# Performance work log

Measured on AMD Instinct MI355X. Metric: run time of the kernel, lower is better.

Reference implementation:

```python
import jax, jax.numpy as jnp
import numpy as np

B, N, FD, HD, G = 32, 512, 768, 384, 3
ALPHA = 0.2  # LeakyReLU slope
NEG = -9e15


def layer_norm(x, g, b, eps=1e-5):
    m = jnp.mean(x, axis=-1, keepdims=True)
    v = jnp.var(x, axis=-1, keepdims=True)
    return (x - m) / jnp.sqrt(v + eps) * g + b


def gat_layer(x, adj, W, a):
    # x: [B,N,FD], adj: [N,N], W: [FD,HD], a: [2*HD]
    h = jnp.einsum('bnf,fd->bnd', x, W)  # [B,N,HD]
    # concat score decomposes: e_ij = lrelu(h_i . a[:HD] + h_j . a[HD:])
    e1 = h @ a[:HD]   # [B,N]
    e2 = h @ a[HD:]   # [B,N]
    e = jax.nn.leaky_relu(e1[:, :, None] + e2[:, None, :], ALPHA)  # [B,N,N]
    e = jnp.where(adj[None] > 0, e, NEG)
    att = jax.nn.softmax(e, axis=2)  # masked softmax over neighbors
    h_prime = jnp.einsum('bij,bjd->bid', att, h)
    return jax.nn.elu(h_prime)  # concat=True -> ELU


def setup_inputs() -> dict:
    key = jax.random.key(0)
    ks = jax.random.split(key, 10)
    s = 0.05
    return {
        'x': jax.random.normal(ks[0], (B, N, FD), jnp.float32),
        'adj': jax.random.randint(ks[1], (G, N, N), 0, 2),
        'W': jax.random.normal(ks[2], (G, FD, HD), jnp.float32) * s,
        'a': jax.random.normal(ks[3], (G, 2 * HD), jnp.float32) * s,
        'log_unc': jnp.zeros((G,), jnp.float32),
        'gate_w': jax.random.normal(ks[4], (FD, G), jnp.float32) * s,
        'gate_b': jnp.zeros((G,), jnp.float32),
        'ln1_g': jnp.ones((HD,), jnp.float32),
        'ln1_b': jnp.zeros((HD,), jnp.float32),
        'w1': jax.random.normal(ks[5], (HD, HD), jnp.float32) * s,
        'b1': jnp.zeros((HD,), jnp.float32),
        'w2': jax.random.normal(ks[6], (HD, FD), jnp.float32) * s,
        'b2': jnp.zeros((FD,), jnp.float32),
        'ln2_g': jnp.ones((FD,), jnp.float32),
        'ln2_b': jnp.zeros((FD,), jnp.float32),
    }


def reference(x, adj, W, a, log_unc, gate_w, gate_b, ln1_g, ln1_b,
              w1, b1, w2, b2, ln2_g, ln2_b):
    # global (uncertainty) weights
    unc = jnp.exp(log_unc)
    attw = jax.nn.softmax(1.0 / (unc + 1e-8))  # [G]
    # content gates from batch-averaged features
    avg = jnp.mean(x, axis=0)                          # [N,FD]
    cg = jax.nn.softmax(avg @ gate_w + gate_b, axis=-1)  # [N,G]
    # per-graph GAT + LayerNorm, vmapped over the G graphs
    gouts = jax.vmap(lambda ad, Wi, ai: layer_norm(gat_layer(x, ad, Wi, ai), ln1_g, ln1_b))(adj, W, a)  # [G,B,N,HD]
    weights = 0.7 * attw[:, None, None, None] + 0.3 * cg.T[:, None, :, None]  # [G,1|B,N,1]
    fused = jnp.sum(weights * gouts, axis=0)  # [B,N,HD]
    # output projection + LayerNorm
    proj = jax.nn.relu(fused @ w1 + b1) @ w2 + b2
    proj = layer_norm(proj, ln2_g, ln2_b)
    # residual gate
    gv = jax.nn.sigmoid(jnp.sum(proj * x, axis=-1, keepdims=True) / np.sqrt(FD).astype(np.float32))
    return gv * x + (1.0 - gv) * proj
```

## Files before the change

### kernel.cpp

```cpp
#include <hip/hip_runtime.h>

typedef unsigned short ushort_t;
typedef unsigned int uint_t;
typedef __bf16 bf16x8 __attribute__((ext_vector_type(8)));
typedef float f32x4 __attribute__((ext_vector_type(4)));
typedef unsigned int u32x4 __attribute__((ext_vector_type(4)));
typedef unsigned short u16x4 __attribute__((ext_vector_type(4)));

#define B_SZ 32
#define N_SZ 512
#define FD_SZ 768
#define HD_SZ 384
#define G_SZ 3
#define M_SZ (B_SZ * N_SZ)
#define ALPHA_LR 0.2f
#define NEGV -9.0e15f
#define VTILE (HD_SZ * 32)

__device__ __forceinline__ float bf2f(ushort_t u) { return __uint_as_float(((uint_t)u) << 16); }
__device__ __forceinline__ ushort_t f2bf(float f) {
  uint_t x = __float_as_uint(f);
  return (ushort_t)((x + 0x7fffu + ((x >> 16) & 1u)) >> 16);
}
__device__ __forceinline__ u32x4 pack8(f32x4 lo, f32x4 hi) {
  union { ushort_t us[8]; u32x4 v; } pk;
  pk.us[0] = f2bf(lo.x); pk.us[1] = f2bf(lo.y); pk.us[2] = f2bf(lo.z); pk.us[3] = f2bf(lo.w);
  pk.us[4] = f2bf(hi.x); pk.us[5] = f2bf(hi.y); pk.us[6] = f2bf(hi.z); pk.us[7] = f2bf(hi.w);
  return pk.v;
}

__global__ __launch_bounds__(256) void transpose_f2b(
    const float* __restrict__ src, ushort_t* __restrict__ dst, int R, int C) {
  size_t total = (size_t)R * C;
  size_t base = (size_t)blockIdx.z * total;
  size_t i = (size_t)blockIdx.x * 256 + threadIdx.x;
  if (i < total) {
    int r = (int)(i / C), c = (int)(i % C);
    dst[base + (size_t)c * R + r] = f2bf(src[base + i]);
  }
}

__global__ __launch_bounds__(256) void cast_f2b(
    const float* __restrict__ src, ushort_t* __restrict__ dst) {
  size_t i = (size_t)blockIdx.x * 256 + threadIdx.x;
  f32x4 v = ((const f32x4*)src)[i];
  u16x4 p;
  p[0] = f2bf(v.x); p[1] = f2bf(v.y); p[2] = f2bf(v.z); p[3] = f2bf(v.w);
  ((u16x4*)dst)[i] = p;
}

__global__ __launch_bounds__(256) void pack_adj(
    const int* __restrict__ adj, uint_t* __restrict__ am) {
  size_t i = (size_t)blockIdx.x * 256 + threadIdx.x;
  unsigned long long mask = __ballot(adj[i] != 0);
  int lane = threadIdx.x & 63;
  if ((lane & 31) == 0) am[i >> 5] = (uint_t)(mask >> (lane & 32));
}

__global__ __launch_bounds__(256) void gate_kernel(
    const float* __restrict__ x, const float* __restrict__ gate_w,
    const float* __restrict__ gate_b, float* __restrict__ cg) {
  int n = blockIdx.x;
  int tid = threadIdx.x;
  float a0 = 0.f, a1 = 0.f, a2 = 0.f;
  for (int f = tid; f < FD_SZ; f += 256) {
    float s = 0.f;
#pragma unroll
    for (int b = 0; b < B_SZ; b++) s += x[((size_t)b * N_SZ + n) * FD_SZ + f];
    float avg = s * (1.0f / B_SZ);
    a0 += avg * gate_w[f * 3 + 0];
    a1 += avg * gate_w[f * 3 + 1];
    a2 += avg * gate_w[f * 3 + 2];
  }
  for (int m = 1; m < 64; m <<= 1) {
    a0 += __shfl_xor(a0, m, 64);
    a1 += __shfl_xor(a1, m, 64);
    a2 += __shfl_xor(a2, m, 64);
  }
  __shared__ float red[3][4];
  int wave = tid >> 6, lane = tid & 63;
  if (lane == 0) { red[0][wave] = a0; red[1][wave] = a1; red[2][wave] = a2; }
  __syncthreads();
  if (tid == 0) {
    float l0 = red[0][0] + red[0][1] + red[0][2] + red[0][3] + gate_b[0];
    float l1 = red[1][0] + red[1][1] + red[1][2] + red[1][3] + gate_b[1];
    float l2 = red[2][0] + red[2][1] + red[2][2] + red[2][3] + gate_b[2];
    float mx = fmaxf(l0, fmaxf(l1, l2));
    float e0 = __expf(l0 - mx), e1 = __expf(l1 - mx), e2 = __expf(l2 - mx);
    float inv = 1.0f / (e0 + e1 + e2);
    cg[n * 3 + 0] = e0 * inv;
    cg[n * 3 + 1] = e1 * inv;
    cg[n * 3 + 2] = e2 * inv;
  }
}

template <bool AF32, bool RELU, bool OUTBF16, bool HASBIAS, bool VFOUT>
__global__ __launch_bounds__(256) void gemm_kernel(
    const void* __restrict__ Av, size_t strideA,
    const ushort_t* __restrict__ Bt, size_t strideB,
    const float* __restrict__ bias,
    void* __restrict__ Cv, size_t strideC,
    int M, int K, int Nc) {
  __shared__ __attribute__((aligned(16))) ushort_t As[128 * 32];
  __shared__ __attribute__((aligned(16))) ushort_t Bs[128 * 32];
  int tid = threadIdx.x, wave = tid >> 6, lane = tid & 63;
  int m0 = blockIdx.y * 128, n0 = blockIdx.x * 128;
  const float* Abf32 = (const float*)Av + (size_t)blockIdx.z * strideA;
  const ushort_t* Abb16 = (const ushort_t*)Av + (size_t)blockIdx.z * strideA;
  const ushort_t* Bb = Bt + (size_t)blockIdx.z * strideB;

  f32x4 acc[4][4];
  f32x4 z4 = {0.f, 0.f, 0.f, 0.f};
#pragma unroll
  for (int i = 0; i < 4; i++)
#pragma unroll
    for (int j = 0; j < 4; j++) acc[i][j] = z4;

  int wm = (wave & 1) * 64, wn = (wave >> 1) * 64;
  int srow = lane >> 2, schk = (lane & 3) * 8;

  for (int kt = 0; kt < K; kt += 32) {
    u32x4 av[2], bv[2];
#pragma unroll
    for (int i = 0; i < 2; i++) {
      int row = m0 + wave * 32 + i * 16 + srow;
      if (AF32) {
        const float* ap = Abf32 + (size_t)row * K + kt + schk;
        f32x4 lo = *(const f32x4*)ap;
        f32x4 hi = *(const f32x4*)(ap + 4);
        av[i] = pack8(lo, hi);
      } else {
        av[i] = *(const u32x4*)(Abb16 + (size_t)row * K + kt + schk);
      }
      bv[i] = *(const u32x4*)(Bb + (size_t)(n0 + wave * 32 + i * 16 + srow) * K + kt + schk);
    }
    __syncthreads();
#pragma unroll
    for (int i = 0; i < 2; i++) {
      int rowBase = wave * 32 + i * 16;
      *(u32x4*)(As + rowBase * 32 + lane * 8) = av[i];
      *(u32x4*)(Bs + rowBase * 32 + lane * 8) = bv[i];
    }
    __syncthreads();
    bf16x8 af[4], bfr[4];
#pragma unroll
    for (int t = 0; t < 4; t++) {
      af[t] = *(const bf16x8*)(As + (wm + t * 16 + (lane & 15)) * 32 + (lane >> 4) * 8);
      bfr[t] = *(const bf16x8*)(Bs + (wn + t * 16 + (lane & 15)) * 32 + (lane >> 4) * 8);
    }
#pragma unroll
    for (int mt = 0; mt < 4; mt++)
#pragma unroll
      for (int nt = 0; nt < 4; nt++)
        acc[mt][nt] = __builtin_amdgcn_mfma_f32_16x16x32_bf16(af[mt], bfr[nt], acc[mt][nt], 0, 0, 0);
  }

  if (VFOUT) {
#pragma unroll
    for (int mt = 0; mt < 4; mt++) {
#pragma unroll
      for (int nt = 0; nt < 4; nt++) {
        int d = n0 + wn + nt * 16 + (lane & 15);
        int gm = m0 + wm + mt * 16 + (lane >> 4) * 4;
        int b = gm >> 9, jt = (gm >> 5) & 15, j2 = gm & 31;
        u16x4 pk;
#pragma unroll
        for (int r2 = 0; r2 < 4; r2++) pk[r2] = f2bf(acc[mt][nt][r2]);
        size_t off = ((size_t)((blockIdx.z * B_SZ + b) * 16 + jt)) * VTILE + (size_t)d * 32 + j2;
        *(u16x4*)((ushort_t*)Cv + off) = pk;
      }
    }
  } else {
#pragma unroll
    for (int mt = 0; mt < 4; mt++) {
#pragma unroll
      for (int nt = 0; nt < 4; nt++) {
        int gn = n0 + wn + nt * 16 + (lane & 15);
        float bvs = HASBIAS ? bias[gn] : 0.f;
#pragma unroll
        for (int r2 = 0; r2 < 4; r2++) {
          int gm = m0 + wm + mt * 16 + (lane >> 4) * 4 + r2;
          float v = acc[mt][nt][r2] + bvs;
          if (RELU) v = v > 0.f ? v : 0.f;
          size_t off = (size_t)blockIdx.z * strideC + (size_t)gm * Nc + gn;
          if (OUTBF16) ((ushort_t*)Cv)[off] = f2bf(v);
          else ((float*)Cv)[off] = v;
        }
      }
    }
  }
}

__global__ __launch_bounds__(256) void e12_kernel(
    const ushort_t* __restrict__ vf, const float* __restrict__ a,
    float* __restrict__ e1, float* __restrict__ e2) {
  __shared__ float a1s[HD_SZ], a2s[HD_SZ];
  int g = blockIdx.y;
  int tid = threadIdx.x;
  for (int i = tid; i < HD_SZ; i += 256) {
    a1s[i] = a[g * 2 * HD_SZ + i];
    a2s[i] = a[g * 2 * HD_SZ + HD_SZ + i];
  }
  __syncthreads();
  int m = blockIdx.x * 256 + tid;
  int b = m >> 9, jt = (m >> 5) & 15, j2 = m & 31;
  const ushort_t* col = vf + ((size_t)((g * B_SZ + b) * 16 + jt)) * VTILE + j2;
  float s1 = 0.f, s2 = 0.f;
  for (int d = 0; d < HD_SZ; d++) {
    float h = bf2f(col[d * 32]);
    s1 += h * a1s[d];
    s2 += h * a2s[d];
  }
  e1[(size_t)g * M_SZ + m] = s1;
  e2[(size_t)g * M_SZ + m] = s2;
}

__global__ __launch_bounds__(512, 4) void attn_kernel(
    const uint_t* __restrict__ adjm, const ushort_t* __restrict__ vf,
    const float* __restrict__ e1, const float* __restrict__ e2,
    const float* __restrict__ cg, const float* __restrict__ log_unc,
    const float* __restrict__ ln1g, const float* __restrict__ ln1b,
    ushort_t* __restrict__ fusedbf) {
  __shared__ __attribute__((aligned(16))) ushort_t Pb[32][520];
  __shared__ float e2s[512];
  __shared__ float e1r[32];
  __shared__ uint_t amS[32][16];
  __shared__ float lng[HD_SZ], lnb[HD_SZ];
  __shared__ float cgr[32][3];
  __shared__ float s1s[32][8], s2s[32][8];

  int tid = threadIdx.x, wave = tid >> 6, lane = tid & 63;
  int quad = lane >> 4, l15 = lane & 15;
  int L = blockIdx.x + (blockIdx.y << 4);
  int b = (L & 7) + ((L >> 7) << 3);
  int i0 = ((L >> 3) & 15) * 32;

  float iv0 = 1.f / (__expf(log_unc[0]) + 1e-8f);
  float iv1 = 1.f / (__expf(log_unc[1]) + 1e-8f);
  float iv2 = 1.f / (__expf(log_unc[2]) + 1e-8f);
  float mxa = fmaxf(iv0, fmaxf(iv1, iv2));
  float w0 = __expf(iv0 - mxa), w1 = __expf(iv1 - mxa), w2 = __expf(iv2 - mxa);
  float wsum = 1.f / (w0 + w1 + w2);
  float attw[3] = {w0 * wsum, w1 * wsum, w2 * wsum};

  if (tid < HD_SZ) {
    lng[tid] = ln1g[tid];
    lnb[tid] = ln1b[tid];
  }
  if (tid < 96) cgr[tid / 3][tid % 3] = cg[(i0 + tid / 3) * 3 + tid % 3];

  float facc[24];
#pragma unroll
  for (int t = 0; t < 24; t++) facc[t] = 0.f;

  for (int g = 0; g < G_SZ; g++) {
    __syncthreads();
    if (tid < 32) e1r[tid] = e1[((size_t)g * B_SZ + b) * N_SZ + i0 + tid];
    amS[tid >> 4][tid & 15] = adjm[((size_t)g * N_SZ + i0 + (tid >> 4)) * 16 + (tid & 15)];
    e2s[tid] = e2[((size_t)g * B_SZ + b) * N_SZ + tid];
    __syncthreads();

#pragma unroll
    for (int rr = 0; rr < 4; rr++) {
      int rw = wave * 4 + rr;
      float e1v = e1r[rw];
      float sv[8];
      float m = -3.0e38f;
#pragma unroll
      for (int jj = 0; jj < 8; jj++) {
        int j = lane + jj * 64;
        float s = e1v + e2s[j];
        s = s > 0.f ? s : ALPHA_LR * s;
        uint_t mw = amS[rw][(lane >> 5) + jj * 2];
        s = ((mw >> (j & 31)) & 1u) ? s : NEGV;
        sv[jj] = s;
        m = fmaxf(m, s);
      }
      for (int msk = 1; msk < 64; msk <<= 1) m = fmaxf(m, __shfl_xor(m, msk, 64));
      float sum = 0.f;
#pragma unroll
      for (int jj = 0; jj < 8; jj++) {
        float e = __expf(sv[jj] - m);
        sv[jj] = e;
        sum += e;
      }
      for (int msk = 1; msk < 64; msk <<= 1) sum += __shfl_xor(sum, msk, 64);
      float inv = 1.0f / sum;
#pragma unroll
      for (int jj = 0; jj < 8; jj++) Pb[rw][lane + jj * 64] = f2bf(sv[jj] * inv);
    }
    __syncthreads();

    f32x4 acc[2][3];
    f32x4 z4 = {0.f, 0.f, 0.f, 0.f};
#pragma unroll
    for (int mt = 0; mt < 2; mt++)
#pragma unroll
      for (int t = 0; t < 3; t++) acc[mt][t] = z4;
    const ushort_t* vbase = vf + ((size_t)(g * B_SZ + b) * 16) * VTILE;
#pragma unroll 2
    for (int j0 = 0; j0 < N_SZ; j0 += 32) {
      const ushort_t* vtile = vbase + (size_t)(j0 >> 5) * VTILE;
      bf16x8 af0 = *(const bf16x8*)(&Pb[l15][j0 + quad * 8]);
      bf16x8 af1 = *(const bf16x8*)(&Pb[16 + l15][j0 + quad * 8]);
#pragma unroll
      for (int t = 0; t < 3; t++) {
        bf16x8 bf = *(const bf16x8*)(vtile + (wave * 48 + t * 16 + l15) * 32 + quad * 8);
        acc[0][t] = __builtin_amdgcn_mfma_f32_16x16x32_bf16(af0, bf, acc[0][t], 0, 0, 0);
        acc[1][t] = __builtin_amdgcn_mfma_f32_16x16x32_bf16(af1, bf, acc[1][t], 0, 0, 0);
      }
    }

    float ps1[2][4], ps2[2][4];
#pragma unroll
    for (int mt = 0; mt < 2; mt++)
#pragma unroll
      for (int r = 0; r < 4; r++) { ps1[mt][r] = 0.f; ps2[mt][r] = 0.f; }
#pragma unroll
    for (int mt = 0; mt < 2; mt++)
#pragma unroll
      for (int t = 0; t < 3; t++)
#pragma unroll
        for (int r = 0; r < 4; r++) {
          float v = acc[mt][t][r];
          v = v > 0.f ? v : __expf(v) - 1.f;
          acc[mt][t][r] = v;
          ps1[mt][r] += v;
          ps2[mt][r] += v * v;
        }
#pragma unroll
    for (int msk = 1; msk < 16; msk <<= 1) {
#pragma unroll
      for (int mt = 0; mt < 2; mt++)
#pragma unroll
        for (int r = 0; r < 4; r++) {
          ps1[mt][r] += __shfl_xor(ps1[mt][r], msk, 64);
          ps2[mt][r] += __shfl_xor(ps2[mt][r], msk, 64);
        }
    }
    if (l15 == 0) {
#pragma unroll
      for (int mt = 0; mt < 2; mt++)
#pragma unroll
        for (int r = 0; r < 4; r++) {
          s1s[mt * 16 + quad * 4 + r][wave] = ps1[mt][r];
          s2s[mt * 16 + quad * 4 + r][wave] = ps2[mt][r];
        }
    }
    __syncthreads();
#pragma unroll
    for (int mt = 0; mt < 2; mt++)
#pragma unroll
      for (int r = 0; r < 4; r++) {
        int row = mt * 16 + quad * 4 + r;
        float S1 = 0.f, S2 = 0.f;
#pragma unroll
        for (int w = 0; w < 8; w++) {
          S1 += s1s[row][w];
          S2 += s2s[row][w];
        }
        float mean = S1 * (1.f / HD_SZ);
        float var = S2 * (1.f / HD_SZ) - mean * mean;
        float rs = rsqrtf(var + 1e-5f);
        float wgt = 0.7f * attw[g] + 0.3f * cgr[row][g];
#pragma unroll
        for (int t = 0; t < 3; t++) {
          int d = wave * 48 + t * 16 + l15;
          facc[mt * 12 + t * 4 + r] += wgt * ((acc[mt][t][r] - mean) * rs * lng[d] + lnb[d]);
        }
      }
  }
#pragma unroll
  for (int mt = 0; mt < 2; mt++)
#pragma unroll
    for (int r = 0; r < 4; r++) {
      size_t rowo = ((size_t)b * N_SZ + i0 + mt * 16 + quad * 4 + r) * HD_SZ;
#pragma unroll
      for (int t = 0; t < 3; t++)
        fusedbf[rowo + wave * 48 + t * 16 + l15] = f2bf(facc[mt * 12 + t * 4 + r]);
    }
}

__global__ __launch_bounds__(256) void final_kernel(
    const ushort_t* __restrict__ projbf, const float* __restrict__ x,
    const float* __restrict__ ln2g, const float* __restrict__ ln2b,
    float* __restrict__ out) {
  int row = blockIdx.x;
  int tid = threadIdx.x, wave = tid >> 6, lane = tid & 63;
  const ushort_t* pr = projbf + (size_t)row * FD_SZ;
  const float* xr = x + (size_t)row * FD_SZ;
  float v[3], xv[3];
  float s1 = 0.f, s2 = 0.f;
#pragma unroll
  for (int k = 0; k < 3; k++) {
    int c = tid + k * 256;
    v[k] = bf2f(pr[c]);
    xv[k] = xr[c];
    s1 += v[k];
    s2 += v[k] * v[k];
  }
  for (int m = 1; m < 64; m <<= 1) {
    s1 += __shfl_xor(s1, m, 64);
    s2 += __shfl_xor(s2, m, 64);
  }
  __shared__ float rs1[4], rs2[4], rdt[4];
  if (lane == 0) { rs1[wave] = s1; rs2[wave] = s2; }
  __syncthreads();
  s1 = rs1[0] + rs1[1] + rs1[2] + rs1[3];
  s2 = rs2[0] + rs2[1] + rs2[2] + rs2[3];
  float mean = s1 * (1.f / FD_SZ);
  float var = s2 * (1.f / FD_SZ) - mean * mean;
  float rstd = rsqrtf(var + 1e-5f);
  float dot = 0.f;
  float pn[3];
#pragma unroll
  for (int k = 0; k < 3; k++) {
    int c = tid + k * 256;
    pn[k] = (v[k] - mean) * rstd * ln2g[c] + ln2b[c];
    dot += pn[k] * xv[k];
  }
  for (int m = 1; m < 64; m <<= 1) dot += __shfl_xor(dot, m, 64);
  if (lane == 0) rdt[wave] = dot;
  __syncthreads();
  dot = rdt[0] + rdt[1] + rdt[2] + rdt[3];
  float gv = 1.f / (1.f + __expf(-dot * (1.0f / 27.712812921102035f)));
#pragma unroll
  for (int k = 0; k < 3; k++) {
    int c = tid + k * 256;
    out[(size_t)row * FD_SZ + c] = gv * xv[k] + (1.f - gv) * pn[k];
  }
}

extern "C" void kernel_launch(void* const* d_in, const int* in_sizes, int n_in,
                              void* d_out, int out_size, void* d_ws, size_t ws_size,
                              hipStream_t stream) {
  (void)in_sizes; (void)n_in; (void)out_size; (void)ws_size;
  const float* x = (const float*)d_in[0];
  const int* adj = (const int*)d_in[1];
  const float* W = (const float*)d_in[2];
  const float* a = (const float*)d_in[3];
  const float* log_unc = (const float*)d_in[4];
  const float* gate_w = (const float*)d_in[5];
  const float* gate_b = (const float*)d_in[6];
  const float* ln1g = (const float*)d_in[7];
  const float* ln1b = (const float*)d_in[8];
  const float* w1 = (const float*)d_in[9];
  const float* b1 = (const float*)d_in[10];
  const float* w2 = (const float*)d_in[11];
  const float* b2 = (const float*)d_in[12];
  const float* ln2g = (const float*)d_in[13];
  const float* ln2b = (const float*)d_in[14];

  char* ws = (char*)d_ws;
  ushort_t* Wt      = (ushort_t*)(ws + 0);
  uint_t*   adjm    = (uint_t*)(ws + 0);
  ushort_t* w1t     = (ushort_t*)(ws + 1769472);
  ushort_t* w2t     = (ushort_t*)(ws + 2064384);
  float*    cg      = (float*)(ws + 2654208);
  float*    e1      = (float*)(ws + 2660352);
  float*    e2      = (float*)(ws + 2856960);
  ushort_t* fusedbf = (ushort_t*)(ws + 3053568);
  ushort_t* vf      = (ushort_t*)(ws + 15636480);
  ushort_t* t1bf    = (ushort_t*)(ws + 15636480);
  ushort_t* projbf  = (ushort_t*)(ws + 28219392);
  ushort_t* xb      = (ushort_t*)d_out;

  cast_f2b<<<dim3((M_SZ * FD_SZ) / 1024), 256, 0, stream>>>(x, xb);

  transpose_f2b<<<dim3(1152, 1, 3), 256, 0, stream>>>(W, Wt, FD_SZ, HD_SZ);
  transpose_f2b<<<dim3(576, 1, 1), 256, 0, stream>>>(w1, w1t, HD_SZ, HD_SZ);
  transpose_f2b<<<dim3(1152, 1, 1), 256, 0, stream>>>(w2, w2t, HD_SZ, FD_SZ);

  gate_kernel<<<dim3(N_SZ), 256, 0, stream>>>(x, gate_w, gate_b, cg);

  gemm_kernel<false, false, true, false, true><<<dim3(3, 128, 3), 256, 0, stream>>>(
      xb, 0, Wt, (size_t)HD_SZ * FD_SZ, nullptr, vf, 0,
      M_SZ, FD_SZ, HD_SZ);

  pack_adj<<<dim3((G_SZ * N_SZ * N_SZ) / 256), 256, 0, stream>>>(adj, adjm);

  e12_kernel<<<dim3(M_SZ / 256, G_SZ), 256, 0, stream>>>(vf, a, e1, e2);

  attn_kernel<<<dim3(N_SZ / 32, B_SZ), 512, 0, stream>>>(
      adjm, vf, e1, e2, cg, log_unc, ln1g, ln1b, fusedbf);

  gemm_kernel<false, true, true, true, false><<<dim3(3, 128, 1), 256, 0, stream>>>(
      fusedbf, 0, w1t, 0, b1, t1bf, 0, M_SZ, HD_SZ, HD_SZ);
  gemm_kernel<false, false, true, true, false><<<dim3(6, 128, 1), 256, 0, stream>>>(
      t1bf, 0, w2t, 0, b2, projbf, 0, M_SZ, HD_SZ, FD_SZ);

  final_kernel<<<dim3(M_SZ), 256, 0, stream>>>(projbf, x, ln2g, ln2b, (float*)d_out);
}
```

Before: 349.0 us.

## Split attention kernel across graphs and reduce partials in a separate pass

The attention kernel now launches one block per (row tile, batch, graph) instead of looping over the three graphs inside each block. Each block writes its weighted, layer-normalised output as a bf16 partial into a per-graph slice of the output buffer, and a new kernel sums the three slices into the fused tensor. This triples the grid to raise occupancy and parallelism, at the cost of extra global memory traffic, an additional launch, and an extra bf16 rounding of each partial before the sum.

```diff
diff --git a/kernel.cpp b/kernel.cpp
--- a/kernel.cpp
+++ b/kernel.cpp
@@ -6,6 +6,7 @@
 typedef float f32x4 __attribute__((ext_vector_type(4)));
 typedef unsigned int u32x4 __attribute__((ext_vector_type(4)));
 typedef unsigned short u16x4 __attribute__((ext_vector_type(4)));
+typedef unsigned short u16x8 __attribute__((ext_vector_type(8)));
 
 #define B_SZ 32
 #define N_SZ 512
@@ -16,6 +17,7 @@
 #define ALPHA_LR 0.2f
 #define NEGV -9.0e15f
 #define VTILE (HD_SZ * 32)
+#define PSLICE ((size_t)M_SZ * HD_SZ)
 
 __device__ __forceinline__ float bf2f(ushort_t u) { return __uint_as_float(((uint_t)u) << 16); }
 __device__ __forceinline__ ushort_t f2bf(float f) {
@@ -220,17 +222,18 @@
     const float* __restrict__ e1, const float* __restrict__ e2,
     const float* __restrict__ cg, const float* __restrict__ log_unc,
     const float* __restrict__ ln1g, const float* __restrict__ ln1b,
-    ushort_t* __restrict__ fusedbf) {
+    ushort_t* __restrict__ pf) {
   __shared__ __attribute__((aligned(16))) ushort_t Pb[32][520];
   __shared__ float e2s[512];
   __shared__ float e1r[32];
   __shared__ uint_t amS[32][16];
   __shared__ float lng[HD_SZ], lnb[HD_SZ];
-  __shared__ float cgr[32][3];
+  __shared__ float cgr[32];
   __shared__ float s1s[32][8], s2s[32][8];
 
   int tid = threadIdx.x, wave = tid >> 6, lane = tid & 63;
   int quad = lane >> 4, l15 = lane & 15;
+  int g = blockIdx.z;
   int L = blockIdx.x + (blockIdx.y << 4);
   int b = (L & 7) + ((L >> 7) << 3);
   int i0 = ((L >> 3) & 15) * 32;
@@ -241,144 +244,143 @@
   float mxa = fmaxf(iv0, fmaxf(iv1, iv2));
   float w0 = __expf(iv0 - mxa), w1 = __expf(iv1 - mxa), w2 = __expf(iv2 - mxa);
   float wsum = 1.f / (w0 + w1 + w2);
-  float attw[3] = {w0 * wsum, w1 * wsum, w2 * wsum};
+  float attwg = (g == 0 ? w0 : (g == 1 ? w1 : w2)) * wsum;
 
   if (tid < HD_SZ) {
     lng[tid] = ln1g[tid];
     lnb[tid] = ln1b[tid];
   }
-  if (tid < 96) cgr[tid / 3][tid % 3] = cg[(i0 + tid / 3) * 3 + tid % 3];
-
-  float facc[24];
-#pragma unroll
-  for (int t = 0; t < 24; t++) facc[t] = 0.f;
-
-  for (int g = 0; g < G_SZ; g++) {
-    __syncthreads();
-    if (tid < 32) e1r[tid] = e1[((size_t)g * B_SZ + b) * N_SZ + i0 + tid];
-    amS[tid >> 4][tid & 15] = adjm[((size_t)g * N_SZ + i0 + (tid >> 4)) * 16 + (tid & 15)];
-    e2s[tid] = e2[((size_t)g * B_SZ + b) * N_SZ + tid];
-    __syncthreads();
-
-#pragma unroll
-    for (int rr = 0; rr < 4; rr++) {
-      int rw = wave * 4 + rr;
-      float e1v = e1r[rw];
-      float sv[8];
-      float m = -3.0e38f;
-#pragma unroll
-      for (int jj = 0; jj < 8; jj++) {
-        int j = lane + jj * 64;
-        float s = e1v + e2s[j];
-        s = s > 0.f ? s : ALPHA_LR * s;
-        uint_t mw = amS[rw][(lane >> 5) + jj * 2];
-        s = ((mw >> (j & 31)) & 1u) ? s : NEGV;
-        sv[jj] = s;
-        m = fmaxf(m, s);
-      }
-      for (int msk = 1; msk < 64; msk <<= 1) m = fmaxf(m, __shfl_xor(m, msk, 64));
-      float sum = 0.f;
-#pragma unroll
-      for (int jj = 0; jj < 8; jj++) {
-        float e = __expf(sv[jj] - m);
-        sv[jj] = e;
-        sum += e;
-      }
-      for (int msk = 1; msk < 64; msk <<= 1) sum += __shfl_xor(sum, msk, 64);
-      float inv = 1.0f / sum;
-#pragma unroll
-      for (int jj = 0; jj < 8; jj++) Pb[rw][lane + jj * 64] = f2bf(sv[jj] * inv);
-    }
-    __syncthreads();
-
-    f32x4 acc[2][3];
-    f32x4 z4 = {0.f, 0.f, 0.f, 0.f};
+  if (tid < 32) {
+    cgr[tid] = cg[(i0 + tid) * 3 + g];
+    e1r[tid] = e1[((size_t)g * B_SZ + b) * N_SZ + i0 + tid];
+  }
+  amS[tid >> 4][tid & 15] = adjm[((size_t)g * N_SZ + i0 + (tid >> 4)) * 16 + (tid & 15)];
+  e2s[tid] = e2[((size_t)g * B_SZ + b) * N_SZ + tid];
+  __syncthreads();
+
+#pragma unroll
+  for (int rr = 0; rr < 4; rr++) {
+    int rw = wave * 4 + rr;
+    float e1v = e1r[rw];
+    float sv[8];
+    float m = -3.0e38f;
+#pragma unroll
+    for (int jj = 0; jj < 8; jj++) {
+      int j = lane + jj * 64;
+      float s = e1v + e2s[j];
+      s = s > 0.f ? s : ALPHA_LR * s;
+      uint_t mw = amS[rw][(lane >> 5) + jj * 2];
+      s = ((mw >> (j & 31)) & 1u) ? s : NEGV;
+      sv[jj] = s;
+      m = fmaxf(m, s);
+    }
+    for (int msk = 1; msk < 64; msk <<= 1) m = fmaxf(m, __shfl_xor(m, msk, 64));
+    float sum = 0.f;
+#pragma unroll
+    for (int jj = 0; jj < 8; jj++) {
+      float e = __expf(sv[jj] - m);
+      sv[jj] = e;
+      sum += e;
+    }
+    for (int msk = 1; msk < 64; msk <<= 1) sum += __shfl_xor(sum, msk, 64);
+    float inv = 1.0f / sum;
+#pragma unroll
+    for (int jj = 0; jj < 8; jj++) Pb[rw][lane + jj * 64] = f2bf(sv[jj] * inv);
+  }
+  __syncthreads();
+
+  f32x4 acc[2][3];
+  f32x4 z4 = {0.f, 0.f, 0.f, 0.f};
+#pragma unroll
+  for (int mt = 0; mt < 2; mt++)
+#pragma unroll
+    for (int t = 0; t < 3; t++) acc[mt][t] = z4;
+  const ushort_t* vbase = vf + ((size_t)(g * B_SZ + b) * 16) * VTILE;
+#pragma unroll 2
+  for (int j0 = 0; j0 < N_SZ; j0 += 32) {
+    const ushort_t* vtile = vbase + (size_t)(j0 >> 5) * VTILE;
+    bf16x8 af0 = *(const bf16x8*)(&Pb[l15][j0 + quad * 8]);
+    bf16x8 af1 = *(const bf16x8*)(&Pb[16 + l15][j0 + quad * 8]);
+#pragma unroll
+    for (int t = 0; t < 3; t++) {
+      bf16x8 bf = *(const bf16x8*)(vtile + (wave * 48 + t * 16 + l15) * 32 + quad * 8);
+      acc[0][t] = __builtin_amdgcn_mfma_f32_16x16x32_bf16(af0, bf, acc[0][t], 0, 0, 0);
+      acc[1][t] = __builtin_amdgcn_mfma_f32_16x16x32_bf16(af1, bf, acc[1][t], 0, 0, 0);
+    }
+  }
+
+  float ps1[2][4], ps2[2][4];
+#pragma unroll
+  for (int mt = 0; mt < 2; mt++)
+#pragma unroll
+    for (int r = 0; r < 4; r++) { ps1[mt][r] = 0.f; ps2[mt][r] = 0.f; }
+#pragma unroll
+  for (int mt = 0; mt < 2; mt++)
+#pragma unroll
+    for (int t = 0; t < 3; t++)
+#pragma unroll
+      for (int r = 0; r < 4; r++) {
+        float v = acc[mt][t][r];
+        v = v > 0.f ? v : __expf(v) - 1.f;
+        acc[mt][t][r] = v;
+        ps1[mt][r] += v;
+        ps2[mt][r] += v * v;
+      }
+#pragma unroll
+  for (int msk = 1; msk < 16; msk <<= 1) {
 #pragma unroll
     for (int mt = 0; mt < 2; mt++)
 #pragma unroll
-      for (int t = 0; t < 3; t++) acc[mt][t] = z4;
-    const ushort_t* vbase = vf + ((size_t)(g * B_SZ + b) * 16) * VTILE;
-#pragma unroll 2
-    for (int j0 = 0; j0 < N_SZ; j0 += 32) {
-      const ushort_t* vtile = vbase + (size_t)(j0 >> 5) * VTILE;
-      bf16x8 af0 = *(const bf16x8*)(&Pb[l15][j0 + quad * 8]);
-      bf16x8 af1 = *(const bf16x8*)(&Pb[16 + l15][j0 + quad * 8]);
+      for (int r = 0; r < 4; r++) {
+        ps1[mt][r] += __shfl_xor(ps1[mt][r], msk, 64);
+        ps2[mt][r] += __shfl_xor(ps2[mt][r], msk, 64);
+      }
+  }
+  if (l15 == 0) {
+#pragma unroll
+    for (int mt = 0; mt < 2; mt++)
+#pragma unroll
+      for (int r = 0; r < 4; r++) {
+        s1s[mt * 16 + quad * 4 + r][wave] = ps1[mt][r];
+        s2s[mt * 16 + quad * 4 + r][wave] = ps2[mt][r];
+      }
+  }
+  __syncthreads();
+#pragma unroll
+  for (int mt = 0; mt < 2; mt++)
+#pragma unroll
+    for (int r = 0; r < 4; r++) {
+      int row = mt * 16 + quad * 4 + r;
+      float S1 = 0.f, S2 = 0.f;
+#pragma unroll
+      for (int w = 0; w < 8; w++) {
+        S1 += s1s[row][w];
+        S2 += s2s[row][w];
+      }
+      float mean = S1 * (1.f / HD_SZ);
+      float var = S2 * (1.f / HD_SZ) - mean * mean;
+      float rs = rsqrtf(var + 1e-5f);
+      float wgt = 0.7f * attwg + 0.3f * cgr[row];
+      size_t rowo = (size_t)g * PSLICE + ((size_t)b * N_SZ + i0 + row) * HD_SZ;
 #pragma unroll
       for (int t = 0; t < 3; t++) {
-        bf16x8 bf = *(const bf16x8*)(vtile + (wave * 48 + t * 16 + l15) * 32 + quad * 8);
-        acc[0][t] = __builtin_amdgcn_mfma_f32_16x16x32_bf16(af0, bf, acc[0][t], 0, 0, 0);
-        acc[1][t] = __builtin_amdgcn_mfma_f32_16x16x32_bf16(af1, bf, acc[1][t], 0, 0, 0);
-      }
-    }
-
-    float ps1[2][4], ps2[2][4];
-#pragma unroll
-    for (int mt = 0; mt < 2; mt++)
-#pragma unroll
-      for (int r = 0; r < 4; r++) { ps1[mt][r] = 0.f; ps2[mt][r] = 0.f; }
-#pragma unroll
-    for (int mt = 0; mt < 2; mt++)
-#pragma unroll
-      for (int t = 0; t < 3; t++)
-#pragma unroll
-        for (int r = 0; r < 4; r++) {
-          float v = acc[mt][t][r];
-          v = v > 0.f ? v : __expf(v) - 1.f;
-          acc[mt][t][r] = v;
-          ps1[mt][r] += v;
-          ps2[mt][r] += v * v;
-        }
-#pragma unroll
-    for (int msk = 1; msk < 16; msk <<= 1) {
-#pragma unroll
-      for (int mt = 0; mt < 2; mt++)
-#pragma unroll
-        for (int r = 0; r < 4; r++) {
-          ps1[mt][r] += __shfl_xor(ps1[mt][r], msk, 64);
-          ps2[mt][r] += __shfl_xor(ps2[mt][r], msk, 64);
-        }
-    }
-    if (l15 == 0) {
-#pragma unroll
-      for (int mt = 0; mt < 2; mt++)
-#pragma unroll
-        for (int r = 0; r < 4; r++) {
-          s1s[mt * 16 + quad * 4 + r][wave] = ps1[mt][r];
-          s2s[mt * 16 + quad * 4 + r][wave] = ps2[mt][r];
-        }
-    }
-    __syncthreads();
-#pragma unroll
-    for (int mt = 0; mt < 2; mt++)
-#pragma unroll
-      for (int r = 0; r < 4; r++) {
-        int row = mt * 16 + quad * 4 + r;
-        float S1 = 0.f, S2 = 0.f;
-#pragma unroll
-        for (int w = 0; w < 8; w++) {
-          S1 += s1s[row][w];
-          S2 += s2s[row][w];
-        }
-        float mean = S1 * (1.f / HD_SZ);
-        float var = S2 * (1.f / HD_SZ) - mean * mean;
-        float rs = rsqrtf(var + 1e-5f);
-        float wgt = 0.7f * attw[g] + 0.3f * cgr[row][g];
-#pragma unroll
-        for (int t = 0; t < 3; t++) {
-          int d = wave * 48 + t * 16 + l15;
-          facc[mt * 12 + t * 4 + r] += wgt * ((acc[mt][t][r] - mean) * rs * lng[d] + lnb[d]);
-        }
-      }
-  }
-#pragma unroll
-  for (int mt = 0; mt < 2; mt++)
-#pragma unroll
-    for (int r = 0; r < 4; r++) {
-      size_t rowo = ((size_t)b * N_SZ + i0 + mt * 16 + quad * 4 + r) * HD_SZ;
-#pragma unroll
-      for (int t = 0; t < 3; t++)
-        fusedbf[rowo + wave * 48 + t * 16 + l15] = f2bf(facc[mt * 12 + t * 4 + r]);
-    }
+        int d = wave * 48 + t * 16 + l15;
+        pf[rowo + d] = f2bf(wgt * ((acc[mt][t][r] - mean) * rs * lng[d] + lnb[d]));
+      }
+    }
+}
+
+__global__ __launch_bounds__(256) void reduce3_kernel(
+    const ushort_t* __restrict__ pf, ushort_t* __restrict__ fused) {
+  size_t u = ((size_t)blockIdx.x * 256 + threadIdx.x) * 8;
+  u16x8 a = *(const u16x8*)(pf + u);
+  u16x8 b = *(const u16x8*)(pf + PSLICE + u);
+  u16x8 c = *(const u16x8*)(pf + 2 * PSLICE + u);
+  u16x8 o;
+#pragma unroll
+  for (int k = 0; k < 8; k++)
+    o[k] = f2bf(bf2f(a[k]) + bf2f(b[k]) + bf2f(c[k]));
+  *(u16x8*)(fused + u) = o;
 }
 
 __global__ __launch_bounds__(256) void final_kernel(
@@ -464,6 +466,7 @@
   ushort_t* t1bf    = (ushort_t*)(ws + 15636480);
   ushort_t* projbf  = (ushort_t*)(ws + 28219392);
   ushort_t* xb      = (ushort_t*)d_out;
+  ushort_t* pf      = (ushort_t*)d_out;
 
   cast_f2b<<<dim3((M_SZ * FD_SZ) / 1024), 256, 0, stream>>>(x, xb);
 
@@ -481,8 +484,10 @@
 
   e12_kernel<<<dim3(M_SZ / 256, G_SZ), 256, 0, stream>>>(vf, a, e1, e2);
 
-  attn_kernel<<<dim3(N_SZ / 32, B_SZ), 512, 0, stream>>>(
-      adjm, vf, e1, e2, cg, log_unc, ln1g, ln1b, fusedbf);
+  attn_kernel<<<dim3(N_SZ / 32, B_SZ, G_SZ), 512, 0, stream>>>(
+      adjm, vf, e1, e2, cg, log_unc, ln1g, ln1b, pf);
+
+  reduce3_kernel<<<dim3((M_SZ * HD_SZ) / (256 * 8)), 256, 0, stream>>>(pf, fusedbf);
 
   gemm_kernel<false, true, true, true, false><<<dim3(3, 128, 1), 256, 0, stream>>>(
       fusedbf, 0, w1t, 0, b1, t1bf, 0, M_SZ, HD_SZ, HD_SZ);
```

New measurement: 341.2 us. 1.02x faster.
